# Kernel optimization log

Measured on AMD Instinct MI355X. Metric: run time of the kernel, lower is better.

## Reference

```python
import jax, jax.numpy as jnp
import numpy as np

N, K = 100000, 16
IN, H, OUT = 128, 256, 128
EPS = 1e-5
NEG_SLOPE = 0.2


def _bn(x, gamma, beta):
    # training-mode BatchNorm1d: biased batch stats over dim 0
    m = jnp.mean(x, axis=0)
    v = jnp.mean(jnp.square(x - m), axis=0)
    return (x - m) * jax.lax.rsqrt(v + EPS) * gamma + beta


def _layer(x, W, b, gamma, beta):
    x = x @ W.T + b
    x = jnp.where(x > 0, x, NEG_SLOPE * x)  # LeakyReLU(0.2)
    return _bn(x, gamma, beta)


def setup_inputs() -> dict:
    key = jax.random.key(0)
    ks = jax.random.split(key, 8)
    inp = {
        "input_features": jax.random.normal(ks[0], (N, IN), dtype=jnp.float32),
        "neigh_idx": jax.random.randint(ks[1], (N * K,), 0, N, dtype=jnp.int64 if jax.config.jax_enable_x64 else jnp.int32),
        "prob_retained": 1,
        "W1": jax.random.normal(ks[2], (H, IN), dtype=jnp.float32) * 0.05,
        "b1": jnp.zeros((H,), dtype=jnp.float32),
        "g1": jnp.ones((H,), dtype=jnp.float32),
        "beta1": jnp.zeros((H,), dtype=jnp.float32),
        "W2": jax.random.normal(ks[3], (H, H), dtype=jnp.float32) * 0.05,
        "b2": jnp.zeros((H,), dtype=jnp.float32),
        "g2": jnp.ones((H,), dtype=jnp.float32),
        "beta2": jnp.zeros((H,), dtype=jnp.float32),
        "W3": jax.random.normal(ks[4], (OUT, H), dtype=jnp.float32) * 0.05,
        "b3": jnp.zeros((OUT,), dtype=jnp.float32),
        "g3": jnp.ones((OUT,), dtype=jnp.float32),
        "beta3": jnp.zeros((OUT,), dtype=jnp.float32),
    }
    return inp


def reference(input_features, neigh_idx, prob_retained,
              W1, b1, g1, beta1, W2, b2, g2, beta2, W3, b3, g3, beta3):
    # MLP (BN branch, len(x) > 1)
    f = _layer(input_features, W1, b1, g1, beta1)   # [N, H]
    f = _layer(f, W2, b2, g2, beta2)                # [N, H]
    f = _layer(f, W3, b3, g3, beta3)                # [N, OUT]
    # per-node neighbor mean: index_select + mean, fixed degree K
    node_update = f[neigh_idx].reshape(N, K, OUT).mean(axis=1)  # [N, OUT]
    return (node_update, f)
```

## Files before the change

### kernel.cpp

```cpp
#include <hip/hip_runtime.h>
#include <hip/hip_bf16.h>

typedef __bf16 bf16x8 __attribute__((ext_vector_type(8)));
typedef __bf16 bf16x2 __attribute__((ext_vector_type(2)));
typedef float f32x4 __attribute__((ext_vector_type(4)));

#define NROWS 100000
#define NSTRIPS 6250
#define EPS 1e-5f
#define SLOPE 0.2f
#define INVN 1e-5f

__device__ __forceinline__ bf16x8 cvt8(const float* s) {
    float4 x0 = *(const float4*)s, x1 = *(const float4*)(s + 4);
    bf16x8 o;
    o[0] = (__bf16)x0.x; o[1] = (__bf16)x0.y; o[2] = (__bf16)x0.z; o[3] = (__bf16)x0.w;
    o[4] = (__bf16)x1.x; o[5] = (__bf16)x1.y; o[6] = (__bf16)x1.z; o[7] = (__bf16)x1.w;
    return o;
}

template <int KT, int NI, int WAVES, int MINW, int NTOT, bool F32IN>
__global__ __launch_bounds__(WAVES * 64, MINW)
void gemm_stream(const __bf16* __restrict__ A, const float* __restrict__ A32,
                 const __bf16* __restrict__ W, const float* __restrict__ W32,
                 const float* __restrict__ bias, __bf16* __restrict__ Y,
                 float* __restrict__ sum, float* __restrict__ sumsq)
{
    constexpr int KS = KT / 32;
    const int wave = threadIdx.x >> 6, lane = threadIdx.x & 63;
    const int quad = lane >> 4, l16 = lane & 15;
    const int c0 = blockIdx.y * (NI * 16 * WAVES) + wave * (NI * 16);

    bf16x8 bfrag[NI][KS];
    float bcol[NI];
    #pragma unroll
    for (int ni = 0; ni < NI; ++ni) {
        int col = c0 + ni * 16 + l16;
        bcol[ni] = bias[col];
        #pragma unroll
        for (int ks = 0; ks < KS; ++ks) {
            int k = ks * 32 + quad * 8;
            if constexpr (F32IN) bfrag[ni][ks] = cvt8(W32 + (size_t)col * KT + k);
            else                 bfrag[ni][ks] = *(const bf16x8*)(W + (size_t)col * KT + k);
        }
    }

    float csum[NI] = {}, csq[NI] = {};

    for (int s = blockIdx.x; s < NSTRIPS; s += gridDim.x) {
        int row0 = s * 16;
        bf16x8 afrag[KS];
        #pragma unroll
        for (int ks = 0; ks < KS; ++ks) {
            int k = ks * 32 + quad * 8;
            if constexpr (F32IN) afrag[ks] = cvt8(A32 + (size_t)(row0 + l16) * KT + k);
            else                 afrag[ks] = *(const bf16x8*)(A + (size_t)(row0 + l16) * KT + k);
        }
        f32x4 acc[NI] = {};
        #pragma unroll
        for (int ks = 0; ks < KS; ++ks)
            #pragma unroll
            for (int ni = 0; ni < NI; ++ni)
                acc[ni] = __builtin_amdgcn_mfma_f32_16x16x32_bf16(
                    afrag[ks], bfrag[ni][ks], acc[ni], 0, 0, 0);

        #pragma unroll
        for (int ni = 0; ni < NI; ++ni) {
            int col = c0 + ni * 16 + l16;
            #pragma unroll
            for (int r = 0; r < 4; ++r) {
                float y = acc[ni][r] + bcol[ni];
                y = (y > 0.f) ? y : SLOPE * y;
                Y[(size_t)(row0 + quad * 4 + r) * NTOT + col] = (__bf16)y;
                csum[ni] += y;
                csq[ni]  += y * y;
            }
        }
    }

    #pragma unroll
    for (int ni = 0; ni < NI; ++ni) {
        float s = csum[ni], q = csq[ni];
        s += __shfl_xor(s, 16); s += __shfl_xor(s, 32);
        q += __shfl_xor(q, 16); q += __shfl_xor(q, 32);
        if (quad == 0) {
            int col = c0 + ni * 16 + l16;
            atomicAdd(&sum[col], s);
            atomicAdd(&sumsq[col], q);
        }
    }
}

__global__ void fold_stats_k(const float* __restrict__ sum, const float* __restrict__ sumsq,
                             const float* __restrict__ g, const float* __restrict__ beta,
                             const float* __restrict__ W, const float* __restrict__ b,
                             __bf16* __restrict__ Wf, float* __restrict__ bf_, int K)
{
    __shared__ float s_sh[256], t_sh[256];
    const int n = blockIdx.x, lane = threadIdx.x;
    for (int k = lane; k < K; k += 64) {
        float m = sum[k] * INVN;
        float v = sumsq[k] * INVN - m * m;
        float sc = g[k] * rsqrtf(v + EPS);
        s_sh[k] = sc;
        t_sh[k] = beta[k] - m * sc;
    }
    __syncthreads();
    float dot = 0.f;
    for (int k = lane; k < K; k += 64) {
        float w = W[(size_t)n * K + k];
        Wf[(size_t)n * K + k] = (__bf16)(w * s_sh[k]);
        dot += w * t_sh[k];
    }
    #pragma unroll
    for (int off = 32; off; off >>= 1) dot += __shfl_down(dot, off);
    if (lane == 0) bf_[n] = b[n] + dot;
}

__global__ __launch_bounds__(256)
void finalize_k(const __bf16* __restrict__ Y3, const int* __restrict__ idx,
                const float* __restrict__ sum3, const float* __restrict__ sq3,
                const float* __restrict__ g3, const float* __restrict__ be3,
                float* __restrict__ F, float* __restrict__ out, int N)
{
    const int row = blockIdx.x * 4 + (threadIdx.x >> 6);
    if (row >= N) return;
    const int lane = threadIdx.x & 63;
    const int c = lane * 2;

    const float2 sm = *(const float2*)(sum3 + c);
    const float2 sq = *(const float2*)(sq3 + c);
    const float2 gg = *(const float2*)(g3 + c);
    const float2 bb = *(const float2*)(be3 + c);
    const float m0 = sm.x * INVN, m1 = sm.y * INVN;
    const float v0 = sq.x * INVN - m0 * m0, v1 = sq.y * INVN - m1 * m1;
    const float s0 = gg.x * rsqrtf(v0 + EPS), s1 = gg.y * rsqrtf(v1 + EPS);
    const float t0 = bb.x - m0 * s0, t1 = bb.y - m1 * s1;

    bf16x2 own = *(const bf16x2*)(Y3 + (size_t)row * 128 + c);
    float2 f;
    f.x = (float)own[0] * s0 + t0;
    f.y = (float)own[1] * s1 + t1;
    *(float2*)(F + (size_t)row * 128 + c) = f;

    const int* ib = idx + (size_t)row * 16;
    float a0 = 0.f, a1 = 0.f;
    #pragma unroll
    for (int k = 0; k < 16; ++k) {
        const int j = ib[k];
        bf16x2 v = *(const bf16x2*)(Y3 + (size_t)j * 128 + c);
        a0 += (float)v[0];
        a1 += (float)v[1];
    }
    float2 o;
    o.x = a0 * 0.0625f * s0 + t0;
    o.y = a1 * 0.0625f * s1 + t1;
    *(float2*)(out + (size_t)row * 128 + c) = o;
}

extern "C" void kernel_launch(void* const* d_in, const int* in_sizes, int n_in,
                              void* d_out, int out_size, void* d_ws, size_t ws_size,
                              hipStream_t stream)
{
    const float* X   = (const float*)d_in[0];
    const int*   idx = (const int*)d_in[1];
    const float* W1  = (const float*)d_in[3];
    const float* b1  = (const float*)d_in[4];
    const float* g1  = (const float*)d_in[5];
    const float* be1 = (const float*)d_in[6];
    const float* W2  = (const float*)d_in[7];
    const float* b2  = (const float*)d_in[8];
    const float* g2  = (const float*)d_in[9];
    const float* be2 = (const float*)d_in[10];
    const float* W3  = (const float*)d_in[11];
    const float* b3  = (const float*)d_in[12];
    const float* g3  = (const float*)d_in[13];
    const float* be3 = (const float*)d_in[14];

    char* ws = (char*)d_ws;
    float* sum1 = (float*)(ws + 0);
    float* sq1  = (float*)(ws + 1024);
    float* sum2 = (float*)(ws + 2048);
    float* sq2  = (float*)(ws + 3072);
    float* sum3 = (float*)(ws + 4096);
    float* sq3  = (float*)(ws + 4608);
    float* b2f  = (float*)(ws + 10240);
    float* b3f  = (float*)(ws + 11264);
    __bf16* W2f = (__bf16*)(ws + 13312);
    __bf16* W3f = (__bf16*)(ws + 144384);
    __bf16* Y1  = (__bf16*)(ws + (1 << 20));
    __bf16* Y2  = (__bf16*)(ws + (1 << 20) + 51200000);
    __bf16* Y3  = Y1;

    float* out_nu = (float*)d_out;
    float* F      = out_nu + (size_t)NROWS * 128;

    hipMemsetAsync(d_ws, 0, 5120, stream);

    gemm_stream<128, 2, 4, 4, 256, true><<<dim3(512, 2), 256, 0, stream>>>(
        nullptr, X, nullptr, W1, b1, Y1, sum1, sq1);
    fold_stats_k<<<256, 64, 0, stream>>>(sum1, sq1, g1, be1, W2, b2, W2f, b2f, 256);

    gemm_stream<256, 2, 4, 3, 256, false><<<dim3(384, 2), 256, 0, stream>>>(
        Y1, nullptr, W2f, nullptr, b2f, Y2, sum2, sq2);
    fold_stats_k<<<128, 64, 0, stream>>>(sum2, sq2, g2, be2, W3, b3, W3f, b3f, 256);

    gemm_stream<256, 2, 4, 3, 128, false><<<dim3(768, 1), 256, 0, stream>>>(
        Y2, nullptr, W3f, nullptr, b3f, Y3, sum3, sq3);

    finalize_k<<<25000, 256, 0, stream>>>(Y3, idx, sum3, sq3, g3, be3, F, out_nu, NROWS);
}
```

Before: 390.2 us.

## Stage weight tiles in swizzled LDS instead of per-wave register fragments

```diff
diff --git a/kernel.cpp b/kernel.cpp
--- a/kernel.cpp
+++ b/kernel.cpp
@@ -21,29 +21,37 @@
 
 template <int KT, int NI, int WAVES, int MINW, int NTOT, bool F32IN>
 __global__ __launch_bounds__(WAVES * 64, MINW)
-void gemm_stream(const __bf16* __restrict__ A, const float* __restrict__ A32,
-                 const __bf16* __restrict__ W, const float* __restrict__ W32,
-                 const float* __restrict__ bias, __bf16* __restrict__ Y,
-                 float* __restrict__ sum, float* __restrict__ sumsq)
+void gemm_wlds(const __bf16* __restrict__ A, const float* __restrict__ A32,
+               const __bf16* __restrict__ W, const float* __restrict__ W32,
+               const float* __restrict__ bias, __bf16* __restrict__ Y,
+               float* __restrict__ sum, float* __restrict__ sumsq)
 {
     constexpr int KS = KT / 32;
-    const int wave = threadIdx.x >> 6, lane = threadIdx.x & 63;
+    constexpr int NC = WAVES * NI * 16;
+    constexpr int NTHR = WAVES * 64;
+    constexpr int KC8 = KT / 8;
+    __shared__ __align__(16) char Wsh[NC * KT * 2];
+
+    const int tid = threadIdx.x;
+    const int wave = tid >> 6, lane = tid & 63;
     const int quad = lane >> 4, l16 = lane & 15;
-    const int c0 = blockIdx.y * (NI * 16 * WAVES) + wave * (NI * 16);
-
-    bf16x8 bfrag[NI][KS];
+    const int cb = blockIdx.y * NC;
+    const int c0 = wave * (NI * 16);
+
+    for (int e = tid; e < NC * KC8; e += NTHR) {
+        int c  = e / KC8;
+        int kc = e % KC8;
+        int gcol = cb + c;
+        bf16x8 v;
+        if constexpr (F32IN) v = cvt8(W32 + (size_t)gcol * KT + kc * 8);
+        else                 v = *(const bf16x8*)(W + (size_t)gcol * KT + kc * 8);
+        *(bf16x8*)(Wsh + c * (KT * 2) + ((kc * 16) ^ ((c & 7) << 4))) = v;
+    }
+    __syncthreads();
+
     float bcol[NI];
     #pragma unroll
-    for (int ni = 0; ni < NI; ++ni) {
-        int col = c0 + ni * 16 + l16;
-        bcol[ni] = bias[col];
-        #pragma unroll
-        for (int ks = 0; ks < KS; ++ks) {
-            int k = ks * 32 + quad * 8;
-            if constexpr (F32IN) bfrag[ni][ks] = cvt8(W32 + (size_t)col * KT + k);
-            else                 bfrag[ni][ks] = *(const bf16x8*)(W + (size_t)col * KT + k);
-        }
-    }
+    for (int ni = 0; ni < NI; ++ni) bcol[ni] = bias[cb + c0 + ni * 16 + l16];
 
     float csum[NI] = {}, csq[NI] = {};
 
@@ -58,15 +66,20 @@
         }
         f32x4 acc[NI] = {};
         #pragma unroll
-        for (int ks = 0; ks < KS; ++ks)
+        for (int ks = 0; ks < KS; ++ks) {
+            const int kb = (ks * 32 + quad * 8) * 2;
             #pragma unroll
-            for (int ni = 0; ni < NI; ++ni)
+            for (int ni = 0; ni < NI; ++ni) {
+                const int c = c0 + ni * 16 + l16;
+                bf16x8 bfrag = *(const bf16x8*)(Wsh + c * (KT * 2) + (kb ^ ((c & 7) << 4)));
                 acc[ni] = __builtin_amdgcn_mfma_f32_16x16x32_bf16(
-                    afrag[ks], bfrag[ni][ks], acc[ni], 0, 0, 0);
+                    afrag[ks], bfrag, acc[ni], 0, 0, 0);
+            }
+        }
 
         #pragma unroll
         for (int ni = 0; ni < NI; ++ni) {
-            int col = c0 + ni * 16 + l16;
+            int col = cb + c0 + ni * 16 + l16;
             #pragma unroll
             for (int r = 0; r < 4; ++r) {
                 float y = acc[ni][r] + bcol[ni];
@@ -84,7 +97,7 @@
         s += __shfl_xor(s, 16); s += __shfl_xor(s, 32);
         q += __shfl_xor(q, 16); q += __shfl_xor(q, 32);
         if (quad == 0) {
-            int col = c0 + ni * 16 + l16;
+            int col = cb + c0 + ni * 16 + l16;
             atomicAdd(&sum[col], s);
             atomicAdd(&sumsq[col], q);
         }
@@ -197,15 +210,15 @@
 
     hipMemsetAsync(d_ws, 0, 5120, stream);
 
-    gemm_stream<128, 2, 4, 4, 256, true><<<dim3(512, 2), 256, 0, stream>>>(
+    gemm_wlds<128, 2, 8, 4, 256, true><<<dim3(512, 1), 512, 0, stream>>>(
         nullptr, X, nullptr, W1, b1, Y1, sum1, sq1);
     fold_stats_k<<<256, 64, 0, stream>>>(sum1, sq1, g1, be1, W2, b2, W2f, b2f, 256);
 
-    gemm_stream<256, 2, 4, 3, 256, false><<<dim3(384, 2), 256, 0, stream>>>(
+    gemm_wlds<256, 2, 4, 2, 256, false><<<dim3(512, 2), 256, 0, stream>>>(
         Y1, nullptr, W2f, nullptr, b2f, Y2, sum2, sq2);
     fold_stats_k<<<128, 64, 0, stream>>>(sum2, sq2, g2, be2, W3, b3, W3f, b3f, 256);
 
-    gemm_stream<256, 2, 4, 3, 128, false><<<dim3(768, 1), 256, 0, stream>>>(
+    gemm_wlds<256, 2, 4, 2, 128, false><<<dim3(512, 1), 256, 0, stream>>>(
         Y2, nullptr, W3f, nullptr, b3f, Y3, sum3, sq3);
 
     finalize_k<<<25000, 256, 0, stream>>>(Y3, idx, sum3, sq3, g3, be3, F, out_nu, NROWS);
```

Result: slower. 398.0 us (+2.0%).
